# Kernel tuning notes

Hardware: AMD Instinct MI355X
Metric: run time of the kernel (lower is better)

## Reference

```python
import jax, jax.numpy as jnp
import numpy as np
import math

H = 256; L = 4; ATOM_DIM = 100; TDIM = 128; NF = 10
B = 128; NN = 32; GS = 8
N = B * NN; E = B * NN * NN
DIS = NF * 2 * 3
DIN_E = 2 * H + 6 + DIS + 3
TWO_PI = 2.0 * math.pi

# symmetric 3x3 basis for CrystalFamily.v2m (log-lattice parameterization)
_b = np.zeros((6, 3, 3), np.float32)
_b[0, 0, 0] = 1.; _b[1, 1, 1] = 1.; _b[2, 2, 2] = 1.
_b[3, 0, 1] = _b[3, 1, 0] = 1.; _b[4, 0, 2] = _b[4, 2, 0] = 1.; _b[5, 1, 2] = _b[5, 2, 1] = 1.
BASIS = jnp.asarray(_b)


def _fwd(t, atom_types, frac_coords, lattices, G, k_mean, k_std, k_mask, k_bias,
         emb_w, emb_b, latent_w, latent_b, edge_w1, edge_b1, edge_w2, edge_b2,
         node_w1, node_b1, node_w2, node_b2, coord_w, lattice_w,
         node2graph, inv_G_permutation, group_size):
    # --- gen_edges: fully connected per graph (row-major, self-loops incl.) ---
    i = jnp.arange(NN)
    src_l = jnp.repeat(i, NN); dst_l = jnp.tile(i, NN)
    off = (jnp.arange(B) * NN)[:, None]
    src = (off + src_l[None, :]).reshape(-1)   # [E]
    dst = (off + dst_l[None, :]).reshape(-1)   # [E]
    e2g = jnp.repeat(jnp.arange(B), NN * NN)   # [E]
    # logmap frac diff
    z = TWO_PI * (frac_coords[dst] - frac_coords[src])
    frac_diff = jnp.arctan2(jnp.sin(z), jnp.cos(z)) / TWO_PI  # [E,3]
    # --- compute_frac_lattice_features ---
    y = lattices * k_std + k_mean
    y = y * k_mask + k_bias
    S = jnp.einsum('bk,kij->bij', y, BASIS)                    # [B,3,3]
    Lm = jax.vmap(jax.scipy.linalg.expm)(S)                    # v2m
    ltl = jnp.einsum('bji,bjk->bik', Lm, Lm)                   # L^T L
    ltl_f = jnp.einsum('eij,ej->ei', ltl[e2g], frac_diff)
    l_f = ltl_f / (jnp.linalg.norm(ltl_f, axis=-1, keepdims=True) + 1e-6)  # [E,3]
    # --- sinusoidal distance embedding (detached in original) ---
    freqs = TWO_PI * jnp.arange(NF, dtype=jnp.float32)
    de = (frac_diff[..., None] * freqs).reshape(E, 3 * NF)
    dis = jax.lax.stop_gradient(jnp.concatenate([jnp.sin(de), jnp.cos(de)], axis=-1))  # [E,60]
    # --- node embedding + time ---
    h = atom_types @ emb_w.T + emb_b
    half = TDIM // 2
    tf = jnp.exp(-math.log(10000.0) * jnp.arange(half, dtype=jnp.float32) / half)
    ta = t[:, None] * tf[None]
    temb = jnp.concatenate([jnp.cos(ta), jnp.sin(ta)], axis=-1)  # [B,TDIM] (cos first)
    tpa = jnp.repeat(temb, NN, axis=0)                           # repeat_interleave(num_atoms)
    h = jnp.concatenate([h, tpa], axis=-1) @ latent_w.T + latent_b
    # --- message passing layers ---
    lat_e = lattices[e2g]  # [E,6]
    deg = jax.ops.segment_sum(jnp.ones((E,), jnp.float32), src, num_segments=N)
    inv_deg = 1.0 / jnp.maximum(deg, 1.0)
    for l in range(L):
        ein = jnp.concatenate([h[src], h[dst], lat_e, dis, l_f], axis=-1)  # [E,581]
        ef = jax.nn.silu(ein @ edge_w1[l].T + edge_b1[l])
        ef = jax.nn.silu(ef @ edge_w2[l].T + edge_b2[l])
        agg = jax.ops.segment_sum(ef, src, num_segments=N) * inv_deg[:, None]  # scatter-mean
        nf = jnp.concatenate([h, agg], axis=-1)
        nf = jax.nn.silu(nf @ node_w1[l].T + node_b1[l])
        nf = jax.nn.silu(nf @ node_w2[l].T + node_b2[l])
        h = h + nf  # residual
    # --- heads ---
    graph_feat = jax.ops.segment_sum(h, node2graph, num_segments=B) / NN  # mean pool
    coord = h @ coord_w.T  # [N,3]
    # equivariant split-and-average
    x = coord.reshape(B, NN, 3)
    x = jnp.repeat(x, group_size, axis=0)                                   # [B*g,NN,3]
    x = jnp.take_along_axis(x, inv_G_permutation[:, :, None], axis=1)
    x = jnp.concatenate([x, jnp.ones((B * group_size, NN, 1), x.dtype)], axis=-1)
    zc = jnp.einsum('bni,bji->bnj', x, G)[:, :, :3]
    out_x = zc.reshape(B, group_size, NN, 3).mean(axis=1).reshape(N, 3)
    lattice_out = graph_feat @ lattice_w.T
    return out_x, lattice_out


def setup_inputs() -> dict:
    key = jax.random.key(0)
    ks = jax.random.split(key, 40)
    w = lambda k, s: jax.random.normal(k, s, jnp.float32) * 0.02
    inp = {}
    inp['t'] = jax.random.uniform(ks[0], (B,))
    inp['atom_types'] = jax.random.normal(ks[1], (N, ATOM_DIM))
    inp['frac_coords'] = jax.random.uniform(ks[2], (N, 3))
    inp['lattices'] = jax.random.normal(ks[3], (B, 6)) * 0.1
    inp['G'] = jnp.eye(4)[None] + 0.1 * jax.random.normal(ks[4], (B * GS, 4, 4))
    inp['k_mean'] = jax.random.normal(ks[5], (6,)) * 0.1
    inp['k_std'] = jnp.ones((6,))
    inp['k_mask'] = jnp.ones((6,))
    inp['k_bias'] = jnp.zeros((6,))
    inp['emb_w'] = w(ks[6], (H, ATOM_DIM)); inp['emb_b'] = jnp.zeros((H,))
    inp['latent_w'] = w(ks[7], (H, H + TDIM)); inp['latent_b'] = jnp.zeros((H,))
    inp['edge_w1'] = w(ks[8], (L, H, DIN_E)); inp['edge_b1'] = jnp.zeros((L, H))
    inp['edge_w2'] = w(ks[9], (L, H, H)); inp['edge_b2'] = jnp.zeros((L, H))
    inp['node_w1'] = w(ks[10], (L, H, 2 * H)); inp['node_b1'] = jnp.zeros((L, H))
    inp['node_w2'] = w(ks[11], (L, H, H)); inp['node_b2'] = jnp.zeros((L, H))
    inp['coord_w'] = w(ks[12], (3, H))
    inp['lattice_w'] = w(ks[13], (6, H))
    inp['num_atoms'] = jnp.full((B,), NN, jnp.int32)
    inp['node2graph'] = jnp.repeat(jnp.arange(B, dtype=jnp.int32), NN)
    pk = jax.random.split(ks[14], B * GS)
    inp['inv_G_permutation'] = jax.vmap(lambda k: jax.random.permutation(k, NN))(pk).astype(jnp.int32)
    inp['group_size'] = GS
    inp['tensor_group_size'] = jnp.full((B,), GS, jnp.int32)
    return inp


def reference(t, atom_types, frac_coords, lattices, G, k_mean, k_std, k_mask, k_bias,
              emb_w, emb_b, latent_w, latent_b, edge_w1, edge_b1, edge_w2, edge_b2,
              node_w1, node_b1, node_w2, node_b2, coord_w, lattice_w,
              num_atoms, node2graph, inv_G_permutation, group_size, tensor_group_size):
    return _fwd(t, atom_types, frac_coords, lattices, G, k_mean, k_std, k_mask, k_bias,
                emb_w, emb_b, latent_w, latent_b, edge_w1, edge_b1, edge_w2, edge_b2,
                node_w1, node_b1, node_w2, node_b2, coord_w, lattice_w,
                node2graph, inv_G_permutation, group_size)
```

## Files before the change

### kernel.cpp

```cpp
#include <hip/hip_runtime.h>
#include <math.h>

namespace {
constexpr int kH = 256;
constexpr int kL = 4;
constexpr int kAtomDim = 100;
constexpr int kB = 128;
constexpr int kNN = 32;
constexpr int kGS = 8;
constexpr int kN = kB * kNN;
constexpr int kE = kB * kNN * kNN;
constexpr int kDinE = 581;
constexpr int kKF = 96;
constexpr float kTwoPi = 6.28318530717958647692f;

typedef __bf16 bf16x8 __attribute__((ext_vector_type(8)));
typedef float  f32x4  __attribute__((ext_vector_type(4)));

__device__ __forceinline__ float fsilu(float x) {
    return x * __builtin_amdgcn_rcpf(1.0f + __expf(-x));
}

__global__ void lattice_kernel(const float* __restrict__ lattices,
                               const float* __restrict__ k_mean,
                               const float* __restrict__ k_std,
                               const float* __restrict__ k_mask,
                               const float* __restrict__ k_bias,
                               float* __restrict__ ltl) {
    int b = threadIdx.x;
    if (b >= kB) return;
    double y[6];
    for (int k = 0; k < 6; ++k) {
        double v = (double)lattices[b * 6 + k] * (double)k_std[k] + (double)k_mean[k];
        y[k] = v * (double)k_mask[k] + (double)k_bias[k];
    }
    double A[9] = { y[0], y[3], y[4],
                    y[3], y[1], y[5],
                    y[4], y[5], y[2] };
    double nrm = 0.0;
    for (int i = 0; i < 3; ++i) {
        double r = fabs(A[i*3+0]) + fabs(A[i*3+1]) + fabs(A[i*3+2]);
        nrm = fmax(nrm, r);
    }
    int s = 0;
    while (nrm > 0.25 && s < 40) { nrm *= 0.5; s++; }
    double sc = 1.0;
    for (int i = 0; i < s; ++i) sc *= 0.5;
    for (int i = 0; i < 9; ++i) A[i] *= sc;
    double T[9]    = {1,0,0, 0,1,0, 0,0,1};
    double term[9] = {1,0,0, 0,1,0, 0,0,1};
    for (int it = 1; it <= 18; ++it) {
        double nt[9];
        double inv = 1.0 / (double)it;
        for (int i = 0; i < 3; ++i)
            for (int j = 0; j < 3; ++j) {
                double acc = 0.0;
                for (int k = 0; k < 3; ++k) acc += term[i*3+k] * A[k*3+j];
                nt[i*3+j] = acc * inv;
            }
        for (int i = 0; i < 9; ++i) { term[i] = nt[i]; T[i] += nt[i]; }
    }
    for (int q = 0; q < s; ++q) {
        double nt[9];
        for (int i = 0; i < 3; ++i)
            for (int j = 0; j < 3; ++j) {
                double acc = 0.0;
                for (int k = 0; k < 3; ++k) acc += T[i*3+k] * T[k*3+j];
                nt[i*3+j] = acc;
            }
        for (int i = 0; i < 9; ++i) T[i] = nt[i];
    }
    for (int i = 0; i < 3; ++i)
        for (int k = 0; k < 3; ++k) {
            double acc = 0.0;
            for (int j = 0; j < 3; ++j) acc += T[j*3+i] * T[j*3+k];
            ltl[b*9 + i*3 + k] = (float)acc;
        }
}

__global__ void feats_bf_kernel(const float* __restrict__ frac,
                                const float* __restrict__ lattices,
                                const float* __restrict__ ltl,
                                __bf16* __restrict__ out) {
    int e = blockIdx.x * blockDim.x + threadIdx.x;
    if (e >= kE) return;
    int g = e >> 10;
    int src = (g << 5) + ((e >> 5) & 31);
    int dst = (g << 5) + (e & 31);
    float d[3];
    #pragma unroll
    for (int c = 0; c < 3; ++c) {
        float delta = frac[dst*3 + c] - frac[src*3 + c];
        d[c] = delta - rintf(delta);
    }
    __attribute__((aligned(16))) __bf16 f[kKF];
    #pragma unroll
    for (int k = 0; k < 6; ++k) f[k] = (__bf16)lattices[g*6 + k];
    #pragma unroll
    for (int c = 0; c < 3; ++c) {
        float th = d[c] * kTwoPi;
        float s1 = sinf(th), c1 = cosf(th);
        float sk = 0.0f, ck = 1.0f;
        f[6  + c*10] = (__bf16)0.0f;
        f[36 + c*10] = (__bf16)1.0f;
        #pragma unroll
        for (int fr = 1; fr < 10; ++fr) {
            float ns = sk*c1 + ck*s1;
            float nc = ck*c1 - sk*s1;
            sk = ns; ck = nc;
            f[6  + c*10 + fr] = (__bf16)sk;
            f[36 + c*10 + fr] = (__bf16)ck;
        }
    }
    float v0 = ltl[g*9+0]*d[0] + ltl[g*9+1]*d[1] + ltl[g*9+2]*d[2];
    float v1 = ltl[g*9+3]*d[0] + ltl[g*9+4]*d[1] + ltl[g*9+5]*d[2];
    float v2 = ltl[g*9+6]*d[0] + ltl[g*9+7]*d[1] + ltl[g*9+8]*d[2];
    float nr = sqrtf(v0*v0 + v1*v1 + v2*v2) + 1e-6f;
    f[66] = (__bf16)(v0/nr); f[67] = (__bf16)(v1/nr); f[68] = (__bf16)(v2/nr);
    #pragma unroll
    for (int k = 69; k < kKF; ++k) f[k] = (__bf16)0.0f;
    uint4* dstp = (uint4*)(out + (size_t)e * kKF);
    const uint4* srcp = (const uint4*)f;
    #pragma unroll
    for (int i = 0; i < kKF/8; ++i) dstp[i] = srcp[i];
}

constexpr int kW1abN = 4*512*256;
constexpr int kW1cN  = 4*256*kKF;
constexpr int kW2bN  = 4*256*256;
constexpr int kNw1N  = 4*256*512;
constexpr int kNw2N  = 4*256*256;
constexpr int kAtN   = kN*128;
constexpr int kEmbwN = 256*128;
constexpr int kLatwN = 256*384;
constexpr int kConvTotal = kW1abN + kW1cN + kW2bN + kNw1N + kNw2N + kAtN + kEmbwN + kLatwN;

__global__ void conv_all(const float* __restrict__ edge_w1, const float* __restrict__ edge_w2,
                         const float* __restrict__ node_w1, const float* __restrict__ node_w2,
                         const float* __restrict__ atom, const float* __restrict__ emb_w,
                         const float* __restrict__ latent_w,
                         __bf16* __restrict__ w1ab, __bf16* __restrict__ w1c,
                         __bf16* __restrict__ w2b, __bf16* __restrict__ nw1b,
                         __bf16* __restrict__ nw2b, __bf16* __restrict__ at_bf,
                         __bf16* __restrict__ embwb, __bf16* __restrict__ latwb) {
    int i = blockIdx.x * 256 + threadIdx.x;
    if (i < kW1abN) {
        int l = i >> 17, rem = i & 131071, r = rem >> 8, k = rem & 255;
        float v = (r < 256) ? edge_w1[((size_t)(l*256 + r))*kDinE + k]
                            : edge_w1[((size_t)(l*256 + (r-256)))*kDinE + 256 + k];
        w1ab[i] = (__bf16)v;
        return;
    }
    i -= kW1abN;
    if (i < kW1cN) {
        int l = i / (256*kKF), rem = i - l*256*kKF, n = rem / kKF, k = rem - n*kKF;
        w1c[i] = (__bf16)((k < 69) ? edge_w1[((size_t)(l*256 + n))*kDinE + 512 + k] : 0.0f);
        return;
    }
    i -= kW1cN;
    if (i < kW2bN) { w2b[i] = (__bf16)edge_w2[i]; return; }
    i -= kW2bN;
    if (i < kNw1N) { nw1b[i] = (__bf16)node_w1[i]; return; }
    i -= kNw1N;
    if (i < kNw2N) { nw2b[i] = (__bf16)node_w2[i]; return; }
    i -= kNw2N;
    if (i < kAtN) {
        int n = i >> 7, k = i & 127;
        at_bf[i] = (__bf16)((k < kAtomDim) ? atom[(size_t)n*kAtomDim + k] : 0.0f);
        return;
    }
    i -= kAtN;
    if (i < kEmbwN) {
        int n = i >> 7, k = i & 127;
        embwb[i] = (__bf16)((k < kAtomDim) ? emb_w[(size_t)n*kAtomDim + k] : 0.0f);
        return;
    }
    i -= kEmbwN;
    if (i < kLatwN) { latwb[i] = (__bf16)latent_w[i]; return; }
}

__global__ void temb_kernel(const float* __restrict__ t, __bf16* __restrict__ tecat) {
    int g = blockIdx.x;
    int tid = threadIdx.x;
    float tf = expf(-logf(10000.0f) * (float)(tid & 63) / 64.0f);
    float ta = t[g] * tf;
    float v = (tid < 64) ? cosf(ta) : sinf(ta);
    __bf16 bv = (__bf16)v;
    #pragma unroll
    for (int nl = 0; nl < kNN; ++nl)
        tecat[((size_t)(g*kNN + nl))*384 + 256 + tid] = bv;
}

template<int K, int EPI>
__global__ __launch_bounds__(256) void gemm64(
        const __bf16* __restrict__ A, int lda,
        const __bf16* __restrict__ W, int ldw,
        const float* __restrict__ bias,
        __bf16* __restrict__ outbf, int ldo,
        __bf16* __restrict__ outbf2,
        float* __restrict__ hmaster, __bf16* __restrict__ hcat) {
    constexpr int NC = K / 32;
    __shared__ __bf16 As[2][64*40];
    __shared__ __bf16 Bs[2][64*40];
    int tid = threadIdx.x;
    int lane = tid & 63;
    int wid = tid >> 6;
    int wm = wid >> 1, wn = wid & 1;
    int r16 = lane & 15, g4 = lane >> 4;
    int mbase = blockIdx.x * 64;
    int nbase = blockIdx.y * 64;
    int srow = tid >> 2, sseg = tid & 3;
    const __bf16* agp = A + (size_t)(mbase + srow)*lda + sseg*8;
    const __bf16* wgp = W + (size_t)(nbase + srow)*ldw + sseg*8;
    int woff = srow*40 + sseg*8;

    f32x4 acc[2][2] = {};
    uint4 ra, rb;
    ra = *(const uint4*)(agp);
    rb = *(const uint4*)(wgp);
    *(uint4*)&As[0][woff] = ra;
    *(uint4*)&Bs[0][woff] = rb;
    __syncthreads();
    for (int c = 0; c < NC; ++c) {
        int cur = c & 1;
        if (c + 1 < NC) {
            ra = *(const uint4*)(agp + (c+1)*32);
            rb = *(const uint4*)(wgp + (c+1)*32);
        }
        bf16x8 af[2], bfg[2];
        #pragma unroll
        for (int mt = 0; mt < 2; ++mt)
            af[mt] = *(const bf16x8*)&As[cur][(wm*32 + mt*16 + r16)*40 + g4*8];
        #pragma unroll
        for (int nt = 0; nt < 2; ++nt)
            bfg[nt] = *(const bf16x8*)&Bs[cur][(wn*32 + nt*16 + r16)*40 + g4*8];
        #pragma unroll
        for (int mt = 0; mt < 2; ++mt)
            #pragma unroll
            for (int nt = 0; nt < 2; ++nt)
                acc[mt][nt] = __builtin_amdgcn_mfma_f32_16x16x32_bf16(af[mt], bfg[nt], acc[mt][nt], 0, 0, 0);
        if (c + 1 < NC) {
            int nxt = cur ^ 1;
            *(uint4*)&As[nxt][woff] = ra;
            *(uint4*)&Bs[nxt][woff] = rb;
        }
        __syncthreads();
    }
    #pragma unroll
    for (int mt = 0; mt < 2; ++mt)
        #pragma unroll
        for (int nt = 0; nt < 2; ++nt) {
            int n = nbase + wn*32 + nt*16 + r16;
            #pragma unroll
            for (int r = 0; r < 4; ++r) {
                int m = mbase + wm*32 + mt*16 + g4*4 + r;
                float v = acc[mt][nt][r];
                if (EPI == 0) {
                    if (n < 256) outbf[(size_t)m*256 + n] = (__bf16)(v + bias[n]);
                    else         outbf2[(size_t)m*256 + (n - 256)] = (__bf16)v;
                } else if (EPI == 2) {
                    outbf[(size_t)m*ldo + n] = (__bf16)fsilu(v + bias[n]);
                } else if (EPI == 3) {
                    float hv = hmaster[(size_t)m*256 + n] + fsilu(v + bias[n]);
                    hmaster[(size_t)m*256 + n] = hv;
                    hcat[(size_t)m*512 + n] = (__bf16)hv;
                } else if (EPI == 4) {
                    outbf[(size_t)m*ldo + n] = (__bf16)(v + bias[n]);
                } else if (EPI == 5) {
                    float hv = v + bias[n];
                    hmaster[(size_t)m*256 + n] = hv;
                    hcat[(size_t)m*512 + n] = (__bf16)hv;
                }
            }
        }
}

__global__ __launch_bounds__(256, 3) void fused_edge(
        const __bf16* __restrict__ Sb, const __bf16* __restrict__ Dq,
        const __bf16* __restrict__ fb, const __bf16* __restrict__ w1c,
        const __bf16* __restrict__ w2, const float* __restrict__ b2,
        __bf16* __restrict__ hcat) {
    __shared__ __bf16 Ds[32][264];
    __shared__ __bf16 Ss[2][264];
    __shared__ __bf16 W2s[256][40];
    __shared__ __bf16 As_[64][40];

    int tid = threadIdx.x;
    int lane = tid & 63;
    int w = tid >> 6;
    int sl = w >> 1;
    int ch = w & 1;
    int r16 = lane & 15, g4 = lane >> 4;
    int ebase = blockIdx.x * 64;
    int graph = ebase >> 10;
    int s0 = ebase >> 5;

    bf16x8 fReg[3];
    {
        const __bf16* fp = fb + (size_t)(ebase + sl*32 + ch*16 + r16)*kKF + g4*8;
        fReg[0] = *(const bf16x8*)(fp);
        fReg[1] = *(const bf16x8*)(fp + 32);
        fReg[2] = *(const bf16x8*)(fp + 64);
    }
    {
        int dl = tid >> 3, seg = tid & 7;
        const uint4* src = (const uint4*)(Dq + (size_t)(graph*32 + dl)*256 + seg*32);
        uint4* dst = (uint4*)&Ds[dl][seg*32];
        dst[0] = src[0]; dst[1] = src[1]; dst[2] = src[2]; dst[3] = src[3];
    }
    if (tid < 64) {
        int slr = tid >> 5, c8 = (tid & 31)*8;
        *(uint4*)&Ss[slr][c8] = *(const uint4*)(Sb + (size_t)(s0 + slr)*256 + c8);
    }

    int wrow = tid >> 2, wq = tid & 3;
    f32x4 acc2[2][8] = {};
    for (int nc = 0; nc < 8; ++nc) {
        if (nc) __syncthreads();
        #pragma unroll
        for (int p = 0; p < 4; ++p)
            *(uint4*)&W2s[wrow + p*64][wq*8] =
                *(const uint4*)(w2 + (size_t)(wrow + p*64)*256 + nc*32 + wq*8);
        bf16x8 bg0[3], bg1[3];
        #pragma unroll
        for (int kc = 0; kc < 3; ++kc) {
            bg0[kc] = *(const bf16x8*)(w1c + (size_t)(nc*32 + r16)*kKF + kc*32 + g4*8);
            bg1[kc] = *(const bf16x8*)(w1c + (size_t)(nc*32 + 16 + r16)*kKF + kc*32 + g4*8);
        }
        __syncthreads();

        f32x4 acc1[2] = {};
        #pragma unroll
        for (int kc = 0; kc < 3; ++kc) {
            acc1[0] = __builtin_amdgcn_mfma_f32_16x16x32_bf16(fReg[kc], bg0[kc], acc1[0], 0, 0, 0);
            acc1[1] = __builtin_amdgcn_mfma_f32_16x16x32_bf16(fReg[kc], bg1[kc], acc1[1], 0, 0, 0);
        }
        #pragma unroll
        for (int nt = 0; nt < 2; ++nt) {
            int lc = nt*16 + r16;
            int n  = nc*32 + lc;
            float sv = (float)Ss[sl][n];
            #pragma unroll
            for (int r = 0; r < 4; ++r) {
                int row16 = g4*4 + r;
                float v = acc1[nt][r] + sv + (float)Ds[ch*16 + row16][n];
                As_[sl*32 + ch*16 + row16][lc] = (__bf16)fsilu(v);
            }
        }
        __syncthreads();

        bf16x8 am0 = *(const bf16x8*)&As_[sl*32 + r16][g4*8];
        bf16x8 am1 = *(const bf16x8*)&As_[sl*32 + 16 + r16][g4*8];
        #pragma unroll
        for (int nt = 0; nt < 8; ++nt) {
            bf16x8 bv = *(const bf16x8*)&W2s[ch*128 + nt*16 + r16][g4*8];
            acc2[0][nt] = __builtin_amdgcn_mfma_f32_16x16x32_bf16(am0, bv, acc2[0][nt], 0, 0, 0);
            acc2[1][nt] = __builtin_amdgcn_mfma_f32_16x16x32_bf16(am1, bv, acc2[1][nt], 0, 0, 0);
        }
    }

    const float inv32 = 1.0f / 32.0f;
    #pragma unroll
    for (int nt = 0; nt < 8; ++nt) {
        int col = ch*128 + nt*16 + r16;
        float bb = b2[col];
        float p = 0.f;
        #pragma unroll
        for (int r = 0; r < 4; ++r)
            p += fsilu(acc2[0][nt][r] + bb) + fsilu(acc2[1][nt][r] + bb);
        p += __shfl_xor(p, 16);
        p += __shfl_xor(p, 32);
        if (lane < 16)
            hcat[(size_t)(s0 + sl)*512 + 256 + col] = (__bf16)(p * inv32);
    }
}

__global__ void coord_equiv_kernel(const float* __restrict__ h,
                                   const float* __restrict__ coord_w,
                                   const float* __restrict__ G,
                                   const int* __restrict__ invp,
                                   float* __restrict__ out_x) {
    int b = blockIdx.x;
    int tid = threadIdx.x;
    __shared__ float cd[kNN][4];
    if (tid < kNN*3) {
        int nl = tid / 3, j = tid - nl*3;
        const float* hr = h + (size_t)(b*kNN + nl)*kH;
        const float* wr = coord_w + (size_t)j*kH;
        float acc = 0.f;
        #pragma unroll 4
        for (int k = 0; k < kH; ++k) acc += hr[k]*wr[k];
        cd[nl][j] = acc;
    }
    __syncthreads();
    if (tid < kNN*3) {
        int nl = tid / 3, j = tid - nl*3;
        float acc = 0.f;
        for (int g = 0; g < kGS; ++g) {
            int bg = b*kGS + g;
            int p = invp[bg*kNN + nl];
            const float* Gr = G + (size_t)bg*16 + j*4;
            acc += cd[p][0]*Gr[0] + cd[p][1]*Gr[1] + cd[p][2]*Gr[2] + Gr[3];
        }
        out_x[(size_t)(b*kNN + nl)*3 + j] = acc * (1.0f/kGS);
    }
}

__global__ void graphfeat_kernel(const float* __restrict__ h,
                                 const float* __restrict__ lattice_w,
                                 float* __restrict__ out_lat) {
    int g = blockIdx.x;
    int c = threadIdx.x;
    __shared__ float gf[kH];
    float s = 0.f;
    for (int nl = 0; nl < kNN; ++nl) s += h[(size_t)(g*kNN + nl)*kH + c];
    gf[c] = s * (1.0f/kNN);
    __syncthreads();
    if (c < 6) {
        const float* wr = lattice_w + (size_t)c*kH;
        float acc = 0.f;
        #pragma unroll 4
        for (int k = 0; k < kH; ++k) acc += gf[k]*wr[k];
        out_lat[g*6 + c] = acc;
    }
}

}

extern "C" void kernel_launch(void* const* d_in, const int* in_sizes, int n_in,
                              void* d_out, int out_size, void* d_ws, size_t ws_size,
                              hipStream_t stream) {
    (void)in_sizes; (void)n_in; (void)out_size; (void)ws_size;
    const float* t         = (const float*)d_in[0];
    const float* atom      = (const float*)d_in[1];
    const float* frac      = (const float*)d_in[2];
    const float* lattices  = (const float*)d_in[3];
    const float* G         = (const float*)d_in[4];
    const float* k_mean    = (const float*)d_in[5];
    const float* k_std     = (const float*)d_in[6];
    const float* k_mask    = (const float*)d_in[7];
    const float* k_bias    = (const float*)d_in[8];
    const float* emb_w     = (const float*)d_in[9];
    const float* emb_b     = (const float*)d_in[10];
    const float* latent_w  = (const float*)d_in[11];
    const float* latent_b  = (const float*)d_in[12];
    const float* edge_w1   = (const float*)d_in[13];
    const float* edge_b1   = (const float*)d_in[14];
    const float* edge_w2   = (const float*)d_in[15];
    const float* edge_b2   = (const float*)d_in[16];
    const float* node_w1   = (const float*)d_in[17];
    const float* node_b1   = (const float*)d_in[18];
    const float* node_w2   = (const float*)d_in[19];
    const float* node_b2   = (const float*)d_in[20];
    const float* coord_w   = (const float*)d_in[21];
    const float* lattice_w = (const float*)d_in[22];
    const int*   invp      = (const int*)d_in[25];

    float* out_x   = (float*)d_out;
    float* out_lat = (float*)d_out + kN*3;

    char* base = (char*)d_ws;
    size_t off = 0;
    auto carve = [&](size_t bytes) { char* p = base + off; off += bytes; return p; };
    float*  ltl    = (float*)carve(8192);
    float*  h      = (float*)carve(4194304);
    __bf16* Sbuf   = (__bf16*)carve(2097152);
    __bf16* Dbuf   = (__bf16*)carve(2097152);
    __bf16* hcat   = (__bf16*)carve(4194304);
    __bf16* t1     = (__bf16*)carve(2097152);
    __bf16* fb     = (__bf16*)carve(25165824);
    __bf16* w1ab   = (__bf16*)carve(1048576);
    __bf16* w1c    = (__bf16*)carve(262144);
    __bf16* w2b    = (__bf16*)carve(524288);
    __bf16* nw1b   = (__bf16*)carve(1048576);
    __bf16* nw2b   = (__bf16*)carve(524288);
    __bf16* at_bf  = (__bf16*)carve(1048576);
    __bf16* embwb  = (__bf16*)carve(65536);
    __bf16* latwb  = (__bf16*)carve(196608);
    __bf16* tecat  = (__bf16*)carve(3145728);

    lattice_kernel<<<1, 128, 0, stream>>>(lattices, k_mean, k_std, k_mask, k_bias, ltl);
    feats_bf_kernel<<<kE/256, 256, 0, stream>>>(frac, lattices, ltl, fb);
    conv_all<<<(kConvTotal + 255)/256, 256, 0, stream>>>(
        edge_w1, edge_w2, node_w1, node_w2, atom, emb_w, latent_w,
        w1ab, w1c, w2b, nw1b, nw2b, at_bf, embwb, latwb);
    temb_kernel<<<kB, 128, 0, stream>>>(t, tecat);

    gemm64<128, 4><<<dim3(64, 4), 256, 0, stream>>>(
        at_bf, 128, embwb, 128, emb_b,
        tecat, 384, nullptr, nullptr, nullptr);
    gemm64<384, 5><<<dim3(64, 4), 256, 0, stream>>>(
        tecat, 384, latwb, 384, latent_b,
        nullptr, 0, nullptr, h, hcat);

    for (int l = 0; l < kL; ++l) {
        gemm64<256, 0><<<dim3(64, 8), 256, 0, stream>>>(
            hcat, 512, w1ab + (size_t)l*512*256, 256,
            edge_b1 + l*256, Sbuf, 256, Dbuf, nullptr, nullptr);
        fused_edge<<<2048, 256, 0, stream>>>(
            Sbuf, Dbuf, fb, w1c + (size_t)l*256*kKF,
            w2b + (size_t)l*256*256, edge_b2 + l*256, hcat);
        gemm64<512, 2><<<dim3(64, 4), 256, 0, stream>>>(
            hcat, 512, nw1b + (size_t)l*256*512, 512,
            node_b1 + l*256, t1, 256, nullptr, nullptr, nullptr);
        gemm64<256, 3><<<dim3(64, 4), 256, 0, stream>>>(
            t1, 256, nw2b + (size_t)l*256*256, 256,
            node_b2 + l*256, nullptr, 0, nullptr, h, hcat);
    }
    coord_equiv_kernel<<<kB, 128, 0, stream>>>(h, coord_w, G, invp, out_x);
    graphfeat_kernel<<<kB, 256, 0, stream>>>(h, lattice_w, out_lat);
}
```

Measured before the change: 456.2 us.

## Widen fused_edge hidden-chunk to 64 columns and rebalance first GEMM across warps

```diff
diff --git a/kernel.cpp b/kernel.cpp
--- a/kernel.cpp
+++ b/kernel.cpp
@@ -275,15 +275,15 @@
         }
 }
 
-__global__ __launch_bounds__(256, 3) void fused_edge(
+__global__ __launch_bounds__(256, 2) void fused_edge(
         const __bf16* __restrict__ Sb, const __bf16* __restrict__ Dq,
         const __bf16* __restrict__ fb, const __bf16* __restrict__ w1c,
         const __bf16* __restrict__ w2, const float* __restrict__ b2,
         __bf16* __restrict__ hcat) {
     __shared__ __bf16 Ds[32][264];
     __shared__ __bf16 Ss[2][264];
-    __shared__ __bf16 W2s[256][40];
-    __shared__ __bf16 As_[64][40];
+    __shared__ __bf16 W2s[256][72];
+    __shared__ __bf16 As_[64][72];
 
     int tid = threadIdx.x;
     int lane = tid & 63;
@@ -297,7 +297,7 @@
 
     bf16x8 fReg[3];
     {
-        const __bf16* fp = fb + (size_t)(ebase + sl*32 + ch*16 + r16)*kKF + g4*8;
+        const __bf16* fp = fb + (size_t)(ebase + w*16 + r16)*kKF + g4*8;
         fReg[0] = *(const bf16x8*)(fp);
         fReg[1] = *(const bf16x8*)(fp + 32);
         fReg[2] = *(const bf16x8*)(fp + 64);
@@ -312,50 +312,52 @@
         int slr = tid >> 5, c8 = (tid & 31)*8;
         *(uint4*)&Ss[slr][c8] = *(const uint4*)(Sb + (size_t)(s0 + slr)*256 + c8);
     }
-
-    int wrow = tid >> 2, wq = tid & 3;
+    __syncthreads();
+
     f32x4 acc2[2][8] = {};
-    for (int nc = 0; nc < 8; ++nc) {
+    for (int nc = 0; nc < 4; ++nc) {
         if (nc) __syncthreads();
         #pragma unroll
-        for (int p = 0; p < 4; ++p)
-            *(uint4*)&W2s[wrow + p*64][wq*8] =
-                *(const uint4*)(w2 + (size_t)(wrow + p*64)*256 + nc*32 + wq*8);
-        bf16x8 bg0[3], bg1[3];
-        #pragma unroll
-        for (int kc = 0; kc < 3; ++kc) {
-            bg0[kc] = *(const bf16x8*)(w1c + (size_t)(nc*32 + r16)*kKF + kc*32 + g4*8);
-            bg1[kc] = *(const bf16x8*)(w1c + (size_t)(nc*32 + 16 + r16)*kKF + kc*32 + g4*8);
-        }
-        __syncthreads();
-
-        f32x4 acc1[2] = {};
-        #pragma unroll
-        for (int kc = 0; kc < 3; ++kc) {
-            acc1[0] = __builtin_amdgcn_mfma_f32_16x16x32_bf16(fReg[kc], bg0[kc], acc1[0], 0, 0, 0);
-            acc1[1] = __builtin_amdgcn_mfma_f32_16x16x32_bf16(fReg[kc], bg1[kc], acc1[1], 0, 0, 0);
-        }
-        #pragma unroll
-        for (int nt = 0; nt < 2; ++nt) {
-            int lc = nt*16 + r16;
-            int n  = nc*32 + lc;
-            float sv = (float)Ss[sl][n];
+        for (int p = 0; p < 8; ++p) {
+            int row = (tid >> 3) + p*32;
+            int q = tid & 7;
+            *(uint4*)&W2s[row][q*8] =
+                *(const uint4*)(w2 + (size_t)row*256 + nc*64 + q*8);
+        }
+        #pragma unroll
+        for (int ct = 0; ct < 4; ++ct) {
+            f32x4 acc1 = {};
+            #pragma unroll
+            for (int kc = 0; kc < 3; ++kc) {
+                bf16x8 bg = *(const bf16x8*)(w1c +
+                    (size_t)(nc*64 + ct*16 + r16)*kKF + kc*32 + g4*8);
+                acc1 = __builtin_amdgcn_mfma_f32_16x16x32_bf16(fReg[kc], bg, acc1, 0, 0, 0);
+            }
+            int n_loc = ct*16 + r16;
+            int n = nc*64 + n_loc;
             #pragma unroll
             for (int r = 0; r < 4; ++r) {
-                int row16 = g4*4 + r;
-                float v = acc1[nt][r] + sv + (float)Ds[ch*16 + row16][n];
-                As_[sl*32 + ch*16 + row16][lc] = (__bf16)fsilu(v);
+                int e_loc = w*16 + g4*4 + r;
+                float v = acc1[r] + (float)Ss[e_loc >> 5][n] + (float)Ds[e_loc & 31][n];
+                As_[e_loc][n_loc] = (__bf16)fsilu(v);
             }
         }
         __syncthreads();
 
-        bf16x8 am0 = *(const bf16x8*)&As_[sl*32 + r16][g4*8];
-        bf16x8 am1 = *(const bf16x8*)&As_[sl*32 + 16 + r16][g4*8];
+        bf16x8 am[2][2];
+        #pragma unroll
+        for (int half = 0; half < 2; ++half)
+            #pragma unroll
+            for (int ks = 0; ks < 2; ++ks)
+                am[half][ks] = *(const bf16x8*)&As_[sl*32 + half*16 + r16][ks*32 + g4*8];
         #pragma unroll
         for (int nt = 0; nt < 8; ++nt) {
-            bf16x8 bv = *(const bf16x8*)&W2s[ch*128 + nt*16 + r16][g4*8];
-            acc2[0][nt] = __builtin_amdgcn_mfma_f32_16x16x32_bf16(am0, bv, acc2[0][nt], 0, 0, 0);
-            acc2[1][nt] = __builtin_amdgcn_mfma_f32_16x16x32_bf16(am1, bv, acc2[1][nt], 0, 0, 0);
+            #pragma unroll
+            for (int ks = 0; ks < 2; ++ks) {
+                bf16x8 bv = *(const bf16x8*)&W2s[ch*128 + nt*16 + r16][ks*32 + g4*8];
+                acc2[0][nt] = __builtin_amdgcn_mfma_f32_16x16x32_bf16(am[0][ks], bv, acc2[0][nt], 0, 0, 0);
+                acc2[1][nt] = __builtin_amdgcn_mfma_f32_16x16x32_bf16(am[1][ks], bv, acc2[1][nt], 0, 0, 0);
+            }
         }
     }
 
```

Measured after the change: 494.9 us. 1.08x slower.
